# Kernel optimization log

Measured on AMD Instinct MI355X. Metric: run time of the kernel, lower is better.

Reference implementation:

```python
import jax, jax.numpy as jnp
import numpy as np

B, N, HID, NH = 8, 1024, 1024, 16
HD = HID // NH  # head_dim = 64
MLP = 4 * HID
EPS = 1e-6


def _xavier(key, fan_in, fan_out):
    lim = np.sqrt(6.0 / (fan_in + fan_out))
    return jax.random.uniform(key, (fan_in, fan_out), jnp.float32, -lim, lim)


def setup_inputs() -> dict:
    key = jax.random.key(0)
    ks = jax.random.split(key, 10)
    return {
        "x": jax.random.normal(ks[0], (B, N, HID), jnp.float32),
        "c": jax.random.normal(ks[1], (B, HID), jnp.float32),
        "w_ada": _xavier(ks[2], HID, 6 * HID), "b_ada": jnp.zeros((6 * HID,), jnp.float32),
        "wq": _xavier(ks[3], HID, HID), "bq": jnp.zeros((HID,), jnp.float32),
        "wk": _xavier(ks[4], HID, HID), "bk": jnp.zeros((HID,), jnp.float32),
        "wv": _xavier(ks[5], HID, HID), "bv": jnp.zeros((HID,), jnp.float32),
        "wo": _xavier(ks[6], HID, HID), "bo": jnp.zeros((HID,), jnp.float32),
        "w1": _xavier(ks[7], HID, MLP), "b1": jnp.zeros((MLP,), jnp.float32),
        "w2": _xavier(ks[8], MLP, HID), "b2": jnp.zeros((HID,), jnp.float32),
    }


def _ln(t):
    # LayerNorm, elementwise_affine=False, eps=1e-6
    mu = jnp.mean(t, axis=-1, keepdims=True)
    var = jnp.mean(jnp.square(t - mu), axis=-1, keepdims=True)
    return (t - mu) * jax.lax.rsqrt(var + EPS)


def _modulate(t, shift, scale):
    return t * (1.0 + scale[:, None, :]) + shift[:, None, :]


def reference(x, c, w_ada, b_ada, wq, bq, wk, bk, wv, bv, wo, bo, w1, b1, w2, b2):
    cmod = jax.nn.silu(c) @ w_ada + b_ada  # [B, 6*HID]
    sh_msa, sc_msa, g_msa, sh_mlp, sc_mlp, g_mlp = jnp.split(cmod, 6, axis=-1)

    xm = _modulate(_ln(x), sh_msa, sc_msa)  # [B, N, HID]
    q = (xm @ wq + bq).reshape(B, N, NH, HD)
    k = (xm @ wk + bk).reshape(B, N, NH, HD)
    v = (xm @ wv + bv).reshape(B, N, NH, HD)

    # NOTE: original scales by 1/head_dim (not 1/sqrt(head_dim)), fp32 softmax
    scores = jnp.einsum('bihd,bjhd->bhij', q, k) / HD
    attn = jax.nn.softmax(scores.astype(jnp.float32), axis=-1)
    out = jnp.einsum('bhij,bjhd->bihd', attn, v).astype(v.dtype)
    out = out.reshape(B, N, HID) @ wo + bo

    x = x + g_msa[:, None, :] * out

    xm2 = _modulate(_ln(x), sh_mlp, sc_mlp)
    h = jax.nn.gelu(xm2 @ w1 + b1, approximate=False)  # nn.GELU default = exact
    mlp_out = h @ w2 + b2
    return x + g_mlp[:, None, :] * mlp_out
```

## Files before the change

### kernel.cpp

```cpp
#include <hip/hip_runtime.h>
#include <hip/hip_bf16.h>
#include <cstdint>


typedef __bf16 bf16;
typedef __attribute__((ext_vector_type(8))) __bf16 bf16x8;
typedef __attribute__((ext_vector_type(4))) __bf16 bf16x4;
typedef __attribute__((ext_vector_type(4))) float f32x4;

#define SEQ   1024
#define NHID  1024
#define NHEAD 16
#define HDIM  64
#define CMS   6144

#define GLD16(gp, lp)                                                  \
  __builtin_amdgcn_global_load_lds(                                    \
      (const __attribute__((address_space(1))) void*)(gp),             \
      (__attribute__((address_space(3))) void*)(lp), 16, 0, 0)

struct TP4 { const float* s[4]; bf16* d[4]; };

__global__ __launch_bounds__(256) void transpose_conv4(TP4 p)
{
  __shared__ float tile[32][33];
  const float* __restrict__ src = p.s[blockIdx.z];
  bf16* __restrict__ dst = p.d[blockIdx.z];
  int n0 = blockIdx.x * 32, k0 = blockIdx.y * 32;
  int tx = threadIdx.x & 31, ty = threadIdx.x >> 5;
#pragma unroll
  for (int i = 0; i < 32; i += 8)
    tile[ty + i][tx] = src[(size_t)(k0 + ty + i) * 1024 + n0 + tx];
  __syncthreads();
#pragma unroll
  for (int i = 0; i < 32; i += 8)
    dst[(size_t)(n0 + ty + i) * 1024 + k0 + tx] = (bf16)tile[tx][ty + i];
}

__global__ __launch_bounds__(256) void transpose_conv(
    const float* __restrict__ src, bf16* __restrict__ dst, int K, int N)
{
  __shared__ float tile[32][33];
  int n0 = blockIdx.x * 32, k0 = blockIdx.y * 32;
  int tx = threadIdx.x & 31, ty = threadIdx.x >> 5;
#pragma unroll
  for (int i = 0; i < 32; i += 8)
    tile[ty + i][tx] = src[(size_t)(k0 + ty + i) * N + n0 + tx];
  __syncthreads();
#pragma unroll
  for (int i = 0; i < 32; i += 8)
    dst[(size_t)(n0 + ty + i) * K + k0 + tx] = (bf16)tile[tx][ty + i];
}

__global__ __launch_bounds__(256) void ada_kernel(
    const float* __restrict__ c, const float* __restrict__ w_ada,
    const float* __restrict__ b_ada, float* __restrict__ cmod)
{
  __shared__ float cs[1024];
  int b = blockIdx.y;
  int col = blockIdx.x * 256 + threadIdx.x;
  for (int i = threadIdx.x; i < 1024; i += 256) {
    float cv = c[b * 1024 + i];
    cs[i] = cv / (1.0f + __expf(-cv));
  }
  __syncthreads();
  float acc = b_ada[col];
#pragma unroll 8
  for (int kk = 0; kk < 1024; kk++)
    acc += cs[kk] * w_ada[(size_t)kk * CMS + col];
  cmod[b * CMS + col] = acc;
}

__global__ __launch_bounds__(256) void ln_mod(
    const float* __restrict__ x, const float* __restrict__ cmod,
    bf16* __restrict__ out, int sh_off, int sc_off)
{
  int row = blockIdx.x, b = row >> 10, tid = threadIdx.x;
  const float4* xr = (const float4*)(x + (size_t)row * NHID);
  float4 v = xr[tid];
  float s  = v.x + v.y + v.z + v.w;
  float s2 = v.x * v.x + v.y * v.y + v.z * v.z + v.w * v.w;
#pragma unroll
  for (int off = 32; off; off >>= 1) {
    s  += __shfl_xor(s, off);
    s2 += __shfl_xor(s2, off);
  }
  __shared__ float red1[4], red2[4];
  int wave = tid >> 6, lane = tid & 63;
  if (lane == 0) { red1[wave] = s; red2[wave] = s2; }
  __syncthreads();
  float S  = red1[0] + red1[1] + red1[2] + red1[3];
  float S2 = red2[0] + red2[1] + red2[2] + red2[3];
  float mean = S * (1.0f / NHID);
  float var  = S2 * (1.0f / NHID) - mean * mean;
  float rs   = rsqrtf(var + 1e-6f);
  const float4* shp = (const float4*)(cmod + b * CMS + sh_off);
  const float4* scp = (const float4*)(cmod + b * CMS + sc_off);
  float4 sh4 = shp[tid], sc4 = scp[tid];
  bf16x4 o4;
  o4[0] = (bf16)((v.x - mean) * rs * (1.0f + sc4.x) + sh4.x);
  o4[1] = (bf16)((v.y - mean) * rs * (1.0f + sc4.y) + sh4.y);
  o4[2] = (bf16)((v.z - mean) * rs * (1.0f + sc4.z) + sh4.z);
  o4[3] = (bf16)((v.w - mean) * rs * (1.0f + sc4.w) + sh4.w);
  *(bf16x4*)(out + (size_t)row * NHID + tid * 4) = o4;
}

template <int EPI>
__global__ __launch_bounds__(256) void gemm_bt(
    const bf16* __restrict__ A, const bf16* __restrict__ Bt,
    const float* __restrict__ bias, const float* __restrict__ bias2,
    const float* __restrict__ bias3,
    bf16* __restrict__ outb, bf16* __restrict__ outb2,
    bf16* __restrict__ outb3, float* __restrict__ outf,
    const float* __restrict__ cmod, int gate_off,
    const float* __restrict__ resid,
    int N, int K)
{
  __shared__ __align__(16) bf16 As[128 * 64];
  __shared__ __align__(16) bf16 Bs[128 * 64];
  const int tid = threadIdx.x;

  const int gx = gridDim.x;
  const int lid = blockIdx.y * gx + blockIdx.x;
  const int xcd = lid & 7, slot = lid >> 3;
  const int P = gridDim.y >> 3;
  const int by = xcd * P + slot / gx;
  const int bx = slot % gx;
  const int bm = by * 128, bn = bx * 128;

  const int wave = tid >> 6, lane = tid & 63;
  const int quad = lane >> 4, l16 = lane & 15;
  const int wm = (wave >> 1) * 64, wn = (wave & 1) * 64;

  const int sr = tid >> 3;
  const int sc = tid & 7;

  f32x4 acc[4][4];
#pragma unroll
  for (int i = 0; i < 4; i++)
#pragma unroll
    for (int j = 0; j < 4; j++) acc[i][j] = (f32x4)0.0f;

  for (int k0 = 0; k0 < K; k0 += 64) {
#pragma unroll
    for (int i = 0; i < 4; i++) {
      int r = i * 32 + sr;
      int cg = (sc ^ (r & 7)) * 8;
      bf16* lbase_a = As + (size_t)(i * 256 + (tid & 192)) * 8;
      bf16* lbase_b = Bs + (size_t)(i * 256 + (tid & 192)) * 8;
      GLD16(A  + (size_t)(bm + r) * K + k0 + cg, lbase_a);
      GLD16(Bt + (size_t)(bn + r) * K + k0 + cg, lbase_b);
    }
    __syncthreads();
#pragma unroll
    for (int kk = 0; kk < 2; kk++) {
      bf16x8 af[4], bfr[4];
#pragma unroll
      for (int t = 0; t < 4; t++) {
        int ra = wm + t * 16 + l16;
        int rb = wn + t * 16 + l16;
        int cc = kk * 4 + quad;
        af[t]  = *(const bf16x8*)(As + ra * 64 + ((cc ^ (ra & 7)) * 8));
        bfr[t] = *(const bf16x8*)(Bs + rb * 64 + ((cc ^ (rb & 7)) * 8));
      }
#pragma unroll
      for (int mt = 0; mt < 4; mt++)
#pragma unroll
        for (int nt = 0; nt < 4; nt++)
          acc[mt][nt] = __builtin_amdgcn_mfma_f32_16x16x32_bf16(
              af[mt], bfr[nt], acc[mt][nt], 0, 0, 0);
    }
    __syncthreads();
  }

  const int sel = bn >> 10;
  const float* bp = (EPI == 5)
      ? ((sel == 0) ? bias : (sel == 1) ? bias2 : bias3) : bias;
  bf16* qk_out = (EPI == 5) ? ((sel == 0) ? outb : outb2) : outb;

#pragma unroll
  for (int mt = 0; mt < 4; mt++) {
#pragma unroll
    for (int nt = 0; nt < 4; nt++) {
      int col = bn + wn + nt * 16 + l16;
      int colq = col & 1023;
      float bcol = (EPI == 5) ? bp[colq] : bias[col];
      if (EPI == 5 && sel == 2) {
        bf16x4 o4;
#pragma unroll
        for (int r = 0; r < 4; r++) o4[r] = (bf16)(acc[mt][nt][r] + bcol);
        int row0 = bm + wm + mt * 16 + quad * 4;
        int bb = row0 >> 10;
        *(bf16x4*)(outb3 + ((size_t)bb * NHID + colq) * SEQ + (row0 & 1023)) = o4;
      } else if (EPI == 5) {
#pragma unroll
        for (int r = 0; r < 4; r++) {
          int row = bm + wm + mt * 16 + quad * 4 + r;
          qk_out[(size_t)row * 1024 + colq] = (bf16)(acc[mt][nt][r] + bcol);
        }
      } else {
#pragma unroll
        for (int r = 0; r < 4; r++) {
          int row = bm + wm + mt * 16 + quad * 4 + r;
          float val = acc[mt][nt][r] + bcol;
          if (EPI == 1 || EPI == 3) {
            int bb = row >> 10;
            float g = cmod[bb * CMS + gate_off + col];
            outf[(size_t)row * N + col] =
                resid[(size_t)row * N + col] + g * val;
          } else {
            float u2 = 2.0f * val * (0.7978845608f +
                                     0.0356774081f * val * val);
            float e = __expf(u2);
            float th = 1.0f - 2.0f / (e + 1.0f);
            outb[(size_t)row * N + col] = (bf16)(0.5f * val * (1.0f + th));
          }
        }
      }
    }
  }
}

__global__ __launch_bounds__(256) void attn_mfma(
    const bf16* __restrict__ q, const bf16* __restrict__ k,
    const bf16* __restrict__ vt, bf16* __restrict__ o)
{
  __shared__ __align__(16) bf16 Ks[64 * 64];
  __shared__ __align__(16) bf16 Vs[64 * 64];
  __shared__ __align__(16) bf16 Ps[4][32 * 72];

  int bid = blockIdx.x;
  int qt = bid & 7, h = (bid >> 3) & 15, b = bid >> 7;
  int tid = threadIdx.x, wave = tid >> 6, lane = tid & 63;
  int quad = lane >> 4, l16 = lane & 15;
  int qbase = qt * 128 + wave * 32;

  bf16x8 qf[2][2];
  const bf16* qp = q + ((size_t)(b * SEQ + qbase)) * NHID + h * HDIM;
#pragma unroll
  for (int nt = 0; nt < 2; nt++)
#pragma unroll
    for (int kk = 0; kk < 2; kk++) {
      bf16x8 t = *(const bf16x8*)(qp + (size_t)(nt * 16 + l16) * NHID +
                                  kk * 32 + quad * 8);
#pragma unroll
      for (int j = 0; j < 8; j++) t[j] = (bf16)((float)t[j] * 0.015625f);
      qf[nt][kk] = t;
    }

  f32x4 oacc[4][2];
#pragma unroll
  for (int mt = 0; mt < 4; mt++)
#pragma unroll
    for (int nt = 0; nt < 2; nt++) oacc[mt][nt] = (f32x4)0.0f;
  float m_[2] = {-3.0e38f, -3.0e38f}, l_[2] = {0.0f, 0.0f};

  const bf16* kb = k + ((size_t)(b * SEQ)) * NHID + h * HDIM;
  const bf16* vb = vt + ((size_t)(b * NHID + h * HDIM)) * SEQ;

  const int sr0 = tid >> 3, sc0 = tid & 7;

  for (int kt = 0; kt < 16; kt++) {
    __syncthreads();
#pragma unroll
    for (int i = 0; i < 2; i++) {
      int r = i * 32 + sr0;
      int cg = (sc0 ^ (r & 7)) * 8;
      bf16* lk = Ks + (size_t)(i * 256 + (tid & 192)) * 8;
      bf16* lv = Vs + (size_t)(i * 256 + (tid & 192)) * 8;
      GLD16(kb + (size_t)(kt * 64 + r) * NHID + cg, lk);
      GLD16(vb + (size_t)r * SEQ + kt * 64 + cg, lv);
    }
    __syncthreads();

    f32x4 sacc[4][2];
#pragma unroll
    for (int mt = 0; mt < 4; mt++)
#pragma unroll
      for (int nt = 0; nt < 2; nt++) sacc[mt][nt] = (f32x4)0.0f;
#pragma unroll
    for (int kk = 0; kk < 2; kk++) {
      bf16x8 kf[4];
#pragma unroll
      for (int mt = 0; mt < 4; mt++) {
        int row = mt * 16 + l16;
        kf[mt] = *(const bf16x8*)(Ks + row * 64 +
                                  (((kk * 4 + quad) ^ (row & 7)) * 8));
      }
#pragma unroll
      for (int mt = 0; mt < 4; mt++)
#pragma unroll
        for (int nt = 0; nt < 2; nt++)
          sacc[mt][nt] = __builtin_amdgcn_mfma_f32_16x16x32_bf16(
              kf[mt], qf[nt][kk], sacc[mt][nt], 0, 0, 0);
    }

    float alpha[2];
#pragma unroll
    for (int nt = 0; nt < 2; nt++) {
      float tm = -3.0e38f;
#pragma unroll
      for (int mt = 0; mt < 4; mt++)
#pragma unroll
        for (int r = 0; r < 4; r++) tm = fmaxf(tm, sacc[mt][nt][r]);
      tm = fmaxf(tm, __shfl_xor(tm, 16));
      tm = fmaxf(tm, __shfl_xor(tm, 32));
      float mn = fmaxf(m_[nt], tm);
      alpha[nt] = __expf(m_[nt] - mn);
      m_[nt] = mn;
      float ts = 0.0f;
#pragma unroll
      for (int mt = 0; mt < 4; mt++) {
        bf16x4 pv;
#pragma unroll
        for (int r = 0; r < 4; r++) {
          float p = __expf(sacc[mt][nt][r] - mn);
          ts += p;
          pv[r] = (bf16)p;
        }
        *(bf16x4*)(&Ps[wave][(nt * 16 + l16) * 72 + mt * 16 + quad * 4]) = pv;
      }
      ts += __shfl_xor(ts, 16);
      ts += __shfl_xor(ts, 32);
      l_[nt] = l_[nt] * alpha[nt] + ts;
    }
#pragma unroll
    for (int mt = 0; mt < 4; mt++)
#pragma unroll
      for (int nt = 0; nt < 2; nt++)
#pragma unroll
        for (int r = 0; r < 4; r++) oacc[mt][nt][r] *= alpha[nt];

    __asm__ volatile("s_waitcnt lgkmcnt(0)" ::: "memory");

#pragma unroll
    for (int kk = 0; kk < 2; kk++) {
      bf16x8 vf[4], pf[2];
#pragma unroll
      for (int mt = 0; mt < 4; mt++) {
        int row = mt * 16 + l16;
        vf[mt] = *(const bf16x8*)(Vs + row * 64 +
                                  (((kk * 4 + quad) ^ (row & 7)) * 8));
      }
#pragma unroll
      for (int nt = 0; nt < 2; nt++)
        pf[nt] = *(const bf16x8*)(&Ps[wave][(nt * 16 + l16) * 72 +
                                            kk * 32 + quad * 8]);
#pragma unroll
      for (int mt = 0; mt < 4; mt++)
#pragma unroll
        for (int nt = 0; nt < 2; nt++)
          oacc[mt][nt] = __builtin_amdgcn_mfma_f32_16x16x32_bf16(
              vf[mt], pf[nt], oacc[mt][nt], 0, 0, 0);
    }
  }

#pragma unroll
  for (int nt = 0; nt < 2; nt++) {
    float rl = 1.0f / l_[nt];
#pragma unroll
    for (int mt = 0; mt < 4; mt++) {
      bf16x4 o4;
#pragma unroll
      for (int r = 0; r < 4; r++) o4[r] = (bf16)(oacc[mt][nt][r] * rl);
      *(bf16x4*)(o + ((size_t)(b * SEQ + qbase + nt * 16 + l16)) * NHID +
                 h * HDIM + mt * 16 + quad * 4) = o4;
    }
  }
}

#define OFF_CMOD 0u
#define OFF_WQT  196608u
#define OFF_WKT  (OFF_WQT + 2097152u)
#define OFF_WVT  (OFF_WKT + 2097152u)
#define OFF_WOT  (OFF_WVT + 2097152u)
#define OFF_W1T  (OFF_WOT + 2097152u)
#define OFF_W2T  (OFF_W1T + 8388608u)
#define OFF_X2   (OFF_W2T + 8388608u)
#define OFF_XM2  (OFF_X2  + 33554432u)
#define OFF_POOL (OFF_XM2 + 16777216u)

extern "C" void kernel_launch(void* const* d_in, const int* in_sizes, int n_in,
                              void* d_out, int out_size, void* d_ws, size_t ws_size,
                              hipStream_t stream)
{
  const float* x     = (const float*)d_in[0];
  const float* c     = (const float*)d_in[1];
  const float* w_ada = (const float*)d_in[2];
  const float* b_ada = (const float*)d_in[3];
  const float* wq = (const float*)d_in[4];  const float* bq = (const float*)d_in[5];
  const float* wk = (const float*)d_in[6];  const float* bk = (const float*)d_in[7];
  const float* wv = (const float*)d_in[8];  const float* bv = (const float*)d_in[9];
  const float* wo = (const float*)d_in[10]; const float* bo = (const float*)d_in[11];
  const float* w1 = (const float*)d_in[12]; const float* b1 = (const float*)d_in[13];
  const float* w2 = (const float*)d_in[14]; const float* b2 = (const float*)d_in[15];
  float* out = (float*)d_out;
  char* ws = (char*)d_ws;

  float* cmod = (float*)(ws + OFF_CMOD);
  bf16* wqT = (bf16*)(ws + OFF_WQT);
  bf16* wkT = (bf16*)(ws + OFF_WKT);
  bf16* wvT = (bf16*)(ws + OFF_WVT);
  bf16* woT = (bf16*)(ws + OFF_WOT);
  bf16* w1T = (bf16*)(ws + OFF_W1T);
  bf16* w2T = (bf16*)(ws + OFF_W2T);
  float* x2 = (float*)(ws + OFF_X2);
  bf16* xm2 = (bf16*)(ws + OFF_XM2);
  bf16* xm  = (bf16*)(ws + OFF_POOL);
  bf16* qb  = (bf16*)(ws + OFF_POOL + 16777216u);
  bf16* kb  = (bf16*)(ws + OFF_POOL + 33554432u);
  bf16* vtb = (bf16*)(ws + OFF_POOL + 50331648u);
  bf16* ob  = xm;
  bf16* hb  = xm;

  TP4 tp;
  tp.s[0] = wq; tp.s[1] = wk; tp.s[2] = wv; tp.s[3] = wo;
  tp.d[0] = wqT; tp.d[1] = wkT; tp.d[2] = wvT; tp.d[3] = woT;
  transpose_conv4<<<dim3(32, 32, 4), 256, 0, stream>>>(tp);
  transpose_conv<<<dim3(128, 32), 256, 0, stream>>>(w1, w1T, 1024, 4096);
  transpose_conv<<<dim3(32, 128), 256, 0, stream>>>(w2, w2T, 4096, 1024);

  ada_kernel<<<dim3(24, 8), 256, 0, stream>>>(c, w_ada, b_ada, cmod);

  ln_mod<<<8192, 256, 0, stream>>>(x, cmod, xm, 0, 1024);

  gemm_bt<5><<<dim3(24, 64), 256, 0, stream>>>(
      xm, wqT, bq, bk, bv, qb, kb, vtb, nullptr, nullptr, 0, nullptr,
      1024, 1024);

  attn_mfma<<<1024, 256, 0, stream>>>(qb, kb, vtb, ob);

  gemm_bt<1><<<dim3(8, 64), 256, 0, stream>>>(
      ob, woT, bo, nullptr, nullptr, nullptr, nullptr, nullptr, x2,
      cmod, 2048, x, 1024, 1024);

  ln_mod<<<8192, 256, 0, stream>>>(x2, cmod, xm2, 3072, 4096);

  gemm_bt<2><<<dim3(32, 64), 256, 0, stream>>>(
      xm2, w1T, b1, nullptr, nullptr, hb, nullptr, nullptr, nullptr,
      nullptr, 0, nullptr, 4096, 1024);

  gemm_bt<3><<<dim3(8, 64), 256, 0, stream>>>(
      hb, w2T, b2, nullptr, nullptr, nullptr, nullptr, nullptr, out,
      cmod, 5120, x2, 1024, 4096);
}
```

Before: 593.4 us.

## Switch GEMM to 32x32x16 MFMA tiles and drop XCD-aware block remapping

The GEMM inner loop now uses 32x32x16 bf16 MFMA instructions on 2x2 accumulator tiles per wave instead of 16x16x32 on 4x4 tiles, and the epilogue indexing is rewritten for the 32x32 output layout. This halves the LDS fragment reads per MFMA and issues fewer, larger matrix instructions. The XCD-aware block index swizzle is also removed in favor of plain blockIdx mapping, which may change L2 locality across XCDs. Register pressure and epilogue store patterns also shift.

Measured after the change: 582.7 us. No clear change (-1.8%).

```diff
diff --git a/kernel.cpp b/kernel.cpp
--- a/kernel.cpp
+++ b/kernel.cpp
@@ -7,6 +7,7 @@
 typedef __attribute__((ext_vector_type(8))) __bf16 bf16x8;
 typedef __attribute__((ext_vector_type(4))) __bf16 bf16x4;
 typedef __attribute__((ext_vector_type(4))) float f32x4;
+typedef __attribute__((ext_vector_type(16))) float f32x16;
 
 #define SEQ   1024
 #define NHID  1024
@@ -119,27 +120,20 @@
   __shared__ __align__(16) bf16 As[128 * 64];
   __shared__ __align__(16) bf16 Bs[128 * 64];
   const int tid = threadIdx.x;
-
-  const int gx = gridDim.x;
-  const int lid = blockIdx.y * gx + blockIdx.x;
-  const int xcd = lid & 7, slot = lid >> 3;
-  const int P = gridDim.y >> 3;
-  const int by = xcd * P + slot / gx;
-  const int bx = slot % gx;
-  const int bm = by * 128, bn = bx * 128;
+  const int bm = blockIdx.y * 128, bn = blockIdx.x * 128;
 
   const int wave = tid >> 6, lane = tid & 63;
-  const int quad = lane >> 4, l16 = lane & 15;
+  const int l32 = lane & 31, half = lane >> 5;
   const int wm = (wave >> 1) * 64, wn = (wave & 1) * 64;
 
   const int sr = tid >> 3;
   const int sc = tid & 7;
 
-  f32x4 acc[4][4];
-#pragma unroll
-  for (int i = 0; i < 4; i++)
-#pragma unroll
-    for (int j = 0; j < 4; j++) acc[i][j] = (f32x4)0.0f;
+  f32x16 acc[2][2];
+#pragma unroll
+  for (int i = 0; i < 2; i++)
+#pragma unroll
+    for (int j = 0; j < 2; j++) acc[i][j] = (f32x16)0.0f;
 
   for (int k0 = 0; k0 < K; k0 += 64) {
 #pragma unroll
@@ -153,21 +147,21 @@
     }
     __syncthreads();
 #pragma unroll
-    for (int kk = 0; kk < 2; kk++) {
-      bf16x8 af[4], bfr[4];
-#pragma unroll
-      for (int t = 0; t < 4; t++) {
-        int ra = wm + t * 16 + l16;
-        int rb = wn + t * 16 + l16;
-        int cc = kk * 4 + quad;
+    for (int kk = 0; kk < 4; kk++) {
+      int cc = kk * 2 + half;
+      bf16x8 af[2], bfr[2];
+#pragma unroll
+      for (int t = 0; t < 2; t++) {
+        int ra = wm + t * 32 + l32;
+        int rb = wn + t * 32 + l32;
         af[t]  = *(const bf16x8*)(As + ra * 64 + ((cc ^ (ra & 7)) * 8));
         bfr[t] = *(const bf16x8*)(Bs + rb * 64 + ((cc ^ (rb & 7)) * 8));
       }
 #pragma unroll
-      for (int mt = 0; mt < 4; mt++)
-#pragma unroll
-        for (int nt = 0; nt < 4; nt++)
-          acc[mt][nt] = __builtin_amdgcn_mfma_f32_16x16x32_bf16(
+      for (int mt = 0; mt < 2; mt++)
+#pragma unroll
+        for (int nt = 0; nt < 2; nt++)
+          acc[mt][nt] = __builtin_amdgcn_mfma_f32_32x32x16_bf16(
               af[mt], bfr[nt], acc[mt][nt], 0, 0, 0);
     }
     __syncthreads();
@@ -179,41 +173,45 @@
   bf16* qk_out = (EPI == 5) ? ((sel == 0) ? outb : outb2) : outb;
 
 #pragma unroll
-  for (int mt = 0; mt < 4; mt++) {
-#pragma unroll
-    for (int nt = 0; nt < 4; nt++) {
-      int col = bn + wn + nt * 16 + l16;
+  for (int mt = 0; mt < 2; mt++) {
+#pragma unroll
+    for (int nt = 0; nt < 2; nt++) {
+      int col = bn + wn + nt * 32 + l32;
       int colq = col & 1023;
       float bcol = (EPI == 5) ? bp[colq] : bias[col];
-      if (EPI == 5 && sel == 2) {
-        bf16x4 o4;
-#pragma unroll
-        for (int r = 0; r < 4; r++) o4[r] = (bf16)(acc[mt][nt][r] + bcol);
-        int row0 = bm + wm + mt * 16 + quad * 4;
-        int bb = row0 >> 10;
-        *(bf16x4*)(outb3 + ((size_t)bb * NHID + colq) * SEQ + (row0 & 1023)) = o4;
-      } else if (EPI == 5) {
-#pragma unroll
-        for (int r = 0; r < 4; r++) {
-          int row = bm + wm + mt * 16 + quad * 4 + r;
-          qk_out[(size_t)row * 1024 + colq] = (bf16)(acc[mt][nt][r] + bcol);
-        }
-      } else {
-#pragma unroll
-        for (int r = 0; r < 4; r++) {
-          int row = bm + wm + mt * 16 + quad * 4 + r;
-          float val = acc[mt][nt][r] + bcol;
-          if (EPI == 1 || EPI == 3) {
-            int bb = row >> 10;
-            float g = cmod[bb * CMS + gate_off + col];
-            outf[(size_t)row * N + col] =
-                resid[(size_t)row * N + col] + g * val;
-          } else {
-            float u2 = 2.0f * val * (0.7978845608f +
-                                     0.0356774081f * val * val);
-            float e = __expf(u2);
-            float th = 1.0f - 2.0f / (e + 1.0f);
-            outb[(size_t)row * N + col] = (bf16)(0.5f * val * (1.0f + th));
+#pragma unroll
+      for (int g = 0; g < 4; g++) {
+        int row0 = bm + wm + mt * 32 + g * 8 + half * 4;
+        if (EPI == 5 && sel == 2) {
+          bf16x4 o4;
+#pragma unroll
+          for (int r = 0; r < 4; r++)
+            o4[r] = (bf16)(acc[mt][nt][g * 4 + r] + bcol);
+          int bb = row0 >> 10;
+          *(bf16x4*)(outb3 + ((size_t)bb * NHID + colq) * SEQ +
+                     (row0 & 1023)) = o4;
+        } else if (EPI == 5) {
+#pragma unroll
+          for (int r = 0; r < 4; r++)
+            qk_out[(size_t)(row0 + r) * 1024 + colq] =
+                (bf16)(acc[mt][nt][g * 4 + r] + bcol);
+        } else {
+#pragma unroll
+          for (int r = 0; r < 4; r++) {
+            int row = row0 + r;
+            float val = acc[mt][nt][g * 4 + r] + bcol;
+            if (EPI == 1 || EPI == 3) {
+              int bb = row >> 10;
+              float gg = cmod[bb * CMS + gate_off + col];
+              outf[(size_t)row * N + col] =
+                  resid[(size_t)row * N + col] + gg * val;
+            } else {
+              float u2 = 2.0f * val * (0.7978845608f +
+                                       0.0356774081f * val * val);
+              float e = __expf(u2);
+              float th = 1.0f - 2.0f / (e + 1.0f);
+              outb[(size_t)row * N + col] = (bf16)(0.5f * val * (1.0f + th));
+            }
           }
         }
       }
```
